# Optimization experiments

Hardware: AMD Instinct MI355X
Metric: run time of the kernel (lower is better)

## Reference

```python
import jax, jax.numpy as jnp
import numpy as np

TS = 0.1
ECNUM = 1024
CA1NUM = 1024
CA3NUM = 1024
CA3SIGMA = 5.0
TRACKLEN = 100
ACTNUM = 2
BS = 8192
CUELOC = int(0.1 * TRACKLEN)  # sensory cue injected at this step
NOISE_P = 0.04 * TS           # per-step EC3 spontaneous-spike probability


def _xavier_std(fan_in, fan_out):
    return float(np.sqrt(2.0 / (fan_in + fan_out)))


def setup_inputs() -> dict:
    key = jax.random.key(0)
    ks = jax.random.split(key, 6)
    cue = jax.random.normal(ks[0], (BS, ECNUM), jnp.float32)
    ec5_init = jax.random.uniform(ks[1], (BS, ECNUM), jnp.float32)
    wca3ca1 = jax.random.uniform(ks[2], (CA3NUM, CA1NUM), jnp.float32) * 0.01
    wec3ca1 = jax.random.normal(ks[3], (ECNUM, CA1NUM), jnp.float32) * _xavier_std(ECNUM, CA1NUM)
    wca1ec5 = jax.random.normal(ks[4], (CA1NUM, ECNUM), jnp.float32) * _xavier_std(CA1NUM, ECNUM)
    wca1act = jax.random.normal(ks[5], (CA1NUM, ACTNUM), jnp.float32) * _xavier_std(CA1NUM, ACTNUM)
    ca1bias = jnp.zeros((CA1NUM,), jnp.float32)
    ec5bias = jnp.zeros((ECNUM,), jnp.float32)
    actbias = jnp.zeros((ACTNUM,), jnp.float32)
    return {"cue": cue, "ec5_init": ec5_init, "wca3ca1": wca3ca1,
            "wec3ca1": wec3ca1, "wca1ec5": wca1ec5, "wca1act": wca1act,
            "ca1bias": ca1bias, "ec5bias": ec5bias, "actbias": actbias}


def _forward(cue, ec5_init, wca3ca1, wec3ca1, wca1ec5, wca1act, ca1bias, ec5bias, actbias):
    bs = cue.shape[0]
    dt = cue.dtype
    # CA3 place-cell tuning curves for all positions: (T, ca3num)
    ca3center = jnp.linspace(0.0, TRACKLEN, CA3NUM).astype(dt)
    xs = jnp.arange(TRACKLEN)
    ca3_all = jnp.exp(-((ca3center[None, :] - xs[:, None].astype(dt)) ** 2)
                      / (2.0 * CA3SIGMA ** 2))
    drive = ca3_all @ wca3ca1            # (T, ca1num), precomputed CA3->CA1 drive
    cue_mask = (xs == CUELOC).astype(dt)  # (T,)
    noise_key = jax.random.key(42)

    ec3_0 = jnp.zeros((bs, ECNUM), dt)
    ca1_0 = jnp.zeros((bs, CA1NUM), dt)

    def step(carry, inp):
        ec3, ec5, _ = carry
        d, m, t = inp
        ca1 = jax.nn.relu(d[None, :] * (1.0 + jax.nn.sigmoid(ec3 @ wec3ca1)) - ca1bias)
        ec5 = ec5 + (10.0 * TS) * (ca1 @ wca1ec5) + ec5bias
        ec5 = 0.5 + 0.5 * jax.nn.sigmoid(4.0 * (ec5 - 0.5))
        ec3 = ec5 * ec3 + m * cue
        k = jax.random.fold_in(noise_key, t)
        ec3 = ec3 + 0.2 * jax.random.bernoulli(k, NOISE_P, (bs, ECNUM)).astype(dt)
        return (ec3, ec5, ca1), None

    (ec3, ec5, ca1), _ = jax.lax.scan(step, (ec3_0, ec5_init, ca1_0),
                                      (drive, cue_mask, xs))
    return ca1 @ wca1act + actbias       # (bs, actnum)


def reference(cue, ec5_init, wca3ca1, wec3ca1, wca1ec5, wca1act, ca1bias, ec5bias, actbias):
    return _forward(cue, ec5_init, wca3ca1, wec3ca1, wca1ec5, wca1act,
                    ca1bias, ec5bias, actbias)
```

## Files before the change

### kernel.cpp

```cpp
#include <hip/hip_runtime.h>
#include <stdint.h>

#define BS 8192
#define NDIM 1024
#define T_STEPS 100
#define CUE_T 10
#define BK 64
#define NKT (NDIM / BK)

typedef __attribute__((ext_vector_type(8))) short bf16x8;
typedef __attribute__((ext_vector_type(16))) float f32x16;

__device__ inline uint16_t f32_to_bf16(float f) {
    uint32_t u = __float_as_uint(f);
    uint32_t r = u + 0x7fffu + ((u >> 16) & 1u);
    return (uint16_t)(r >> 16);
}
__device__ inline float bf16_to_f32(uint16_t h) {
    return __uint_as_float(((uint32_t)h) << 16);
}

__host__ __device__ inline uint32_t rotl32_(uint32_t x, uint32_t r) {
    return (x << r) | (x >> (32u - r));
}

__host__ __device__ inline void tf2x32(uint32_t k0, uint32_t k1,
                                       uint32_t x0, uint32_t x1,
                                       uint32_t &o0, uint32_t &o1) {
    uint32_t ks2 = k0 ^ k1 ^ 0x1BD11BDAu;
    x0 += k0; x1 += k1;
#define TF_R4(a,b,c,d) \
    x0 += x1; x1 = rotl32_(x1,(a)); x1 ^= x0; \
    x0 += x1; x1 = rotl32_(x1,(b)); x1 ^= x0; \
    x0 += x1; x1 = rotl32_(x1,(c)); x1 ^= x0; \
    x0 += x1; x1 = rotl32_(x1,(d)); x1 ^= x0;
    TF_R4(13,15,26,6)  x0 += k1;  x1 += ks2 + 1u;
    TF_R4(17,29,16,24) x0 += ks2; x1 += k0 + 2u;
    TF_R4(13,15,26,6)  x0 += k0;  x1 += k1 + 3u;
    TF_R4(17,29,16,24) x0 += k1;  x1 += ks2 + 4u;
    TF_R4(13,15,26,6)  x0 += ks2; x1 += k0 + 5u;
#undef TF_R4
    o0 = x0; o1 = x1;
}

__device__ inline float noise_add(uint32_t k0, uint32_t k1, uint32_t idx) {
    uint32_t o0, o1;
    tf2x32(k0, k1, 0u, idx, o0, o1);
    uint32_t bits = o0 ^ o1;
    float u = __uint_as_float((bits >> 9) | 0x3f800000u) - 1.0f;
    return (u < 0.004f) ? 0.2f : 0.0f;
}

__device__ inline float sigmoidf_(float x) {
    return 1.0f / (1.0f + expf(-x));
}

__device__ __forceinline__ void gload16(const uint16_t* g, uint16_t* l) {
    __builtin_amdgcn_global_load_lds(
        (const __attribute__((address_space(1))) void*)g,
        (__attribute__((address_space(3))) void*)l, 16, 0, 0);
}

__global__ void init_kernel(const float* __restrict__ ec5_init,
                            uint16_t* __restrict__ ec3bf,
                            uint16_t* __restrict__ ec5bf, int n) {
    int i = blockIdx.x * blockDim.x + threadIdx.x;
    if (i < n) { ec3bf[i] = 0; ec5bf[i] = f32_to_bf16(ec5_init[i]); }
}

__global__ __launch_bounds__(256) void drive_kernel(const float* __restrict__ W,
                                                    float* __restrict__ drive) {
    __shared__ float g[4][1024];
    const int t0 = blockIdx.x * 4;
    const int c = blockIdx.y * 256 + threadIdx.x;
    const float stepf = 100.0f / 1023.0f;
    for (int i = threadIdx.x; i < 4096; i += 256) {
        int tt = i >> 10, j = i & 1023;
        float d = stepf * (float)j - (float)(t0 + tt);
        g[tt][j] = expf(-(d * d) * 0.02f);
    }
    __syncthreads();
    float a0 = 0.f, a1 = 0.f, a2 = 0.f, a3 = 0.f;
    for (int j = 0; j < 1024; ++j) {
        float w = W[(size_t)j * NDIM + c];
        a0 = fmaf(g[0][j], w, a0);
        a1 = fmaf(g[1][j], w, a1);
        a2 = fmaf(g[2][j], w, a2);
        a3 = fmaf(g[3][j], w, a3);
    }
    drive[(size_t)(t0 + 0) * NDIM + c] = a0;
    drive[(size_t)(t0 + 1) * NDIM + c] = a1;
    drive[(size_t)(t0 + 2) * NDIM + c] = a2;
    drive[(size_t)(t0 + 3) * NDIM + c] = a3;
}

__global__ __launch_bounds__(256) void wtrans_kernel(const float* __restrict__ W,
                                                     uint16_t* __restrict__ Wt) {
    __shared__ float tile[32][33];
    int k0 = blockIdx.x * 32, n0 = blockIdx.y * 32;
    int tx = threadIdx.x & 31, ty = threadIdx.x >> 5;
    #pragma unroll
    for (int i = 0; i < 32; i += 8)
        tile[ty + i][tx] = W[(size_t)(k0 + ty + i) * NDIM + n0 + tx];
    __syncthreads();
    #pragma unroll
    for (int i = 0; i < 32; i += 8)
        Wt[(size_t)(n0 + ty + i) * NDIM + k0 + tx] = f32_to_bf16(tile[tx][ty + i]);
}

__device__ __forceinline__ void gemm_core(const uint16_t* __restrict__ A,
                                          const uint16_t* __restrict__ Bt,
                                          uint16_t* As, uint16_t* Bs,
                                          f32x16 acc[2][2]) {
    const int tid = threadIdx.x;
    const int wid = tid >> 6, lane = tid & 63;
    const int row0 = blockIdx.x * 128, col0 = blockIdx.y * 128;
    const int srow = lane >> 3;
    const int soff = ((lane & 7) ^ srow) * 8;
    const uint16_t* aS[4]; const uint16_t* bS[4];
    #pragma unroll
    for (int i = 0; i < 4; ++i) {
        int ch = wid * 4 + i;
        aS[i] = A  + (size_t)(row0 + ch * 8 + srow) * NDIM + soff;
        bS[i] = Bt + (size_t)(col0 + ch * 8 + srow) * NDIM + soff;
    }
    const int l31 = lane & 31, l5 = lane >> 5;
    const int wr = wid >> 1, wc = wid & 1;
    int aoff[2][4], boff[2][4];
    #pragma unroll
    for (int m = 0; m < 2; ++m)
        #pragma unroll
        for (int kk = 0; kk < 4; ++kk) {
            int ar = wr * 64 + m * 32 + l31;
            aoff[m][kk] = ar * BK + ((((kk << 1) | l5) ^ (ar & 7)) << 3);
            int br = wc * 64 + m * 32 + l31;
            boff[m][kk] = br * BK + ((((kk << 1) | l5) ^ (br & 7)) << 3);
        }

    #pragma unroll
    for (int i = 0; i < 4; ++i) {
        int ch = wid * 4 + i;
        gload16(aS[i], As + ch * 512);
        gload16(bS[i], Bs + ch * 512);
    }

    for (int kt = 0; kt < NKT; ++kt) {
        const int cur = kt & 1;
        if (kt + 1 < NKT) {
            const int nb = (cur ^ 1) * 8192;
            const int k0n = (kt + 1) * BK;
            #pragma unroll
            for (int i = 0; i < 4; ++i) {
                int ch = wid * 4 + i;
                gload16(aS[i] + k0n, As + nb + ch * 512);
                gload16(bS[i] + k0n, Bs + nb + ch * 512);
            }
            asm volatile("s_waitcnt vmcnt(8)" ::: "memory");
        } else {
            asm volatile("s_waitcnt vmcnt(0)" ::: "memory");
        }
        __builtin_amdgcn_s_barrier();
        __builtin_amdgcn_sched_barrier(0);
        const uint16_t* as = As + cur * 8192;
        const uint16_t* bs = Bs + cur * 8192;
        bf16x8 af[2][4], bfr[2][4];
        #pragma unroll
        for (int m = 0; m < 2; ++m)
            #pragma unroll
            for (int kk = 0; kk < 4; ++kk) {
                af[m][kk]  = *(const bf16x8*)&as[aoff[m][kk]];
                bfr[m][kk] = *(const bf16x8*)&bs[boff[m][kk]];
            }
        #pragma unroll
        for (int kk = 0; kk < 4; ++kk)
            #pragma unroll
            for (int m = 0; m < 2; ++m)
                #pragma unroll
                for (int n = 0; n < 2; ++n)
                    acc[m][n] = __builtin_amdgcn_mfma_f32_32x32x16_bf16(
                        af[m][kk], bfr[n][kk], acc[m][n], 0, 0, 0);
        __builtin_amdgcn_sched_barrier(0);
        __builtin_amdgcn_s_barrier();
    }
}

__device__ __forceinline__ void acc_to_lds(float* lacc, f32x16 acc[2][2]) {
    const int tid = threadIdx.x, wid = tid >> 6, lane = tid & 63;
    const int wr = wid >> 1, wc = wid & 1, l31 = lane & 31, l5 = lane >> 5;
    #pragma unroll
    for (int m = 0; m < 2; ++m)
        #pragma unroll
        for (int n = 0; n < 2; ++n) {
            int c = wc * 64 + n * 32 + l31;
            int chunk = c >> 2, cj = c & 3;
            #pragma unroll
            for (int e = 0; e < 16; ++e) {
                int r = wr * 64 + m * 32 + (e & 3) + ((e >> 2) << 3) + (l5 << 2);
                lacc[r * 128 + ((chunk ^ (r & 31)) << 2) + cj] = acc[m][n][e];
            }
        }
}

__device__ __forceinline__ void acc_read8(const float* lacc, int r, int a,
                                          float4 &v0, float4 &v1) {
    int rb = r & 31;
    v0 = *(const float4*)&lacc[r * 128 + ((((a << 1) | 0) ^ rb) << 2)];
    v1 = *(const float4*)&lacc[r * 128 + ((((a << 1) | 1) ^ rb) << 2)];
}

__global__ __launch_bounds__(256, 2) void gemm1_kernel(
    const uint16_t* __restrict__ ec3bf, const uint16_t* __restrict__ W1t,
    const float* __restrict__ drv, const float* __restrict__ bias,
    uint16_t* __restrict__ ca1bf, float* __restrict__ ca1f, int writef32)
{
    __shared__ __align__(16) uint16_t SM[2][16384];
    uint16_t* As = SM[0];
    uint16_t* Bs = SM[1];
    f32x16 acc[2][2];
    #pragma unroll
    for (int m = 0; m < 2; ++m)
        #pragma unroll
        for (int n = 0; n < 2; ++n)
            acc[m][n] = (f32x16)(0.0f);
    gemm_core(ec3bf, W1t, As, Bs, acc);

    float* lacc = (float*)SM;
    acc_to_lds(lacc, acc);
    __syncthreads();

    const int tid = threadIdx.x;
    const int row0 = blockIdx.x * 128, col0 = blockIdx.y * 128;
    const int a = tid & 15;
    #pragma unroll
    for (int i = 0; i < 8; ++i) {
        int r = (tid >> 4) + i * 16;
        float4 v0, v1;
        acc_read8(lacc, r, a, v0, v1);
        int gc = col0 + a * 8;
        float4 d0 = *(const float4*)&drv[gc];
        float4 d1 = *(const float4*)&drv[gc + 4];
        float4 b0 = *(const float4*)&bias[gc];
        float4 b1 = *(const float4*)&bias[gc + 4];
        size_t off = (size_t)(row0 + r) * NDIM + gc;
        float vout[8];
        #pragma unroll
        for (int j = 0; j < 8; ++j) {
            float accv = j < 4 ? v0[j] : v1[j - 4];
            float dv = j < 4 ? d0[j] : d1[j - 4];
            float bi = j < 4 ? b0[j] : b1[j - 4];
            float s = sigmoidf_(accv);
            float v = dv * (1.0f + s) - bi;
            vout[j] = v > 0.0f ? v : 0.0f;
        }
        bf16x8 pk;
        #pragma unroll
        for (int j = 0; j < 8; ++j) pk[j] = (short)f32_to_bf16(vout[j]);
        *(bf16x8*)&ca1bf[off] = pk;
        if (writef32) {
            float4 f0 = {vout[0], vout[1], vout[2], vout[3]};
            float4 f1 = {vout[4], vout[5], vout[6], vout[7]};
            *(float4*)&ca1f[off] = f0;
            *(float4*)&ca1f[off + 4] = f1;
        }
    }
}

__global__ __launch_bounds__(256, 2) void gemm2_kernel(
    const uint16_t* __restrict__ ca1bf, const uint16_t* __restrict__ W2t,
    const float* __restrict__ cue, const float* __restrict__ bias,
    uint16_t* __restrict__ ec3bf, uint16_t* __restrict__ ec5bf,
    uint32_t k0_, uint32_t k1_, int inject)
{
    __shared__ __align__(16) uint16_t SM[2][16384];
    uint16_t* As = SM[0];
    uint16_t* Bs = SM[1];
    f32x16 acc[2][2];
    #pragma unroll
    for (int m = 0; m < 2; ++m)
        #pragma unroll
        for (int n = 0; n < 2; ++n)
            acc[m][n] = (f32x16)(0.0f);
    gemm_core(ca1bf, W2t, As, Bs, acc);

    float* lacc = (float*)SM;
    acc_to_lds(lacc, acc);
    __syncthreads();

    const int tid = threadIdx.x;
    const int row0 = blockIdx.x * 128, col0 = blockIdx.y * 128;
    const int a = tid & 15;
    #pragma unroll
    for (int i = 0; i < 8; ++i) {
        int r = (tid >> 4) + i * 16;
        float4 v0, v1;
        acc_read8(lacc, r, a, v0, v1);
        int gc = col0 + a * 8;
        size_t off = (size_t)(row0 + r) * NDIM + gc;
        bf16x8 e3v = *(const bf16x8*)&ec3bf[off];
        bf16x8 e5v = *(const bf16x8*)&ec5bf[off];
        float4 b0 = *(const float4*)&bias[gc];
        float4 b1 = *(const float4*)&bias[gc + 4];
        float4 c0 = {0.f,0.f,0.f,0.f}, c1 = {0.f,0.f,0.f,0.f};
        if (inject) {
            c0 = *(const float4*)&cue[off];
            c1 = *(const float4*)&cue[off + 4];
        }
        bf16x8 p3, p5;
        #pragma unroll
        for (int j = 0; j < 8; ++j) {
            float accv = j < 4 ? v0[j] : v1[j - 4];
            float bi = j < 4 ? b0[j] : b1[j - 4];
            float e5 = bf16_to_f32((uint16_t)e5v[j]);
            float e3 = bf16_to_f32((uint16_t)e3v[j]);
            float u = e5 + accv + bi;
            float e5n = 0.5f + 0.5f * sigmoidf_(4.0f * (u - 0.5f));
            float e3n = e5n * e3;
            if (inject) e3n += (j < 4 ? c0[j] : c1[j - 4]);
            e3n += noise_add(k0_, k1_, (uint32_t)off + j);
            p5[j] = (short)f32_to_bf16(e5n);
            p3[j] = (short)f32_to_bf16(e3n);
        }
        *(bf16x8*)&ec5bf[off] = p5;
        *(bf16x8*)&ec3bf[off] = p3;
    }
}

__global__ __launch_bounds__(256) void final_kernel(
    const float* __restrict__ ca1,
    const float* __restrict__ wact,
    const float* __restrict__ actbias,
    float* __restrict__ out)
{
    int wave = threadIdx.x >> 6, lane = threadIdx.x & 63;
    int b = blockIdx.x * 4 + wave;
    double a0 = 0.0, a1 = 0.0;
    for (int c = lane; c < NDIM; c += 64) {
        double v = (double)ca1[(size_t)b * NDIM + c];
        a0 += v * (double)wact[c * 2 + 0];
        a1 += v * (double)wact[c * 2 + 1];
    }
    #pragma unroll
    for (int off = 32; off > 0; off >>= 1) {
        a0 += __shfl_down(a0, off);
        a1 += __shfl_down(a1, off);
    }
    if (lane == 0) {
        out[(size_t)b * 2 + 0] = (float)(a0 + (double)actbias[0]);
        out[(size_t)b * 2 + 1] = (float)(a1 + (double)actbias[1]);
    }
}

extern "C" void kernel_launch(void* const* d_in, const int* in_sizes, int n_in,
                              void* d_out, int out_size, void* d_ws, size_t ws_size,
                              hipStream_t stream) {
    const float* cue      = (const float*)d_in[0];
    const float* ec5_init = (const float*)d_in[1];
    const float* wca3ca1  = (const float*)d_in[2];
    const float* wec3ca1  = (const float*)d_in[3];
    const float* wca1ec5  = (const float*)d_in[4];
    const float* wca1act  = (const float*)d_in[5];
    const float* ca1bias  = (const float*)d_in[6];
    const float* ec5bias  = (const float*)d_in[7];
    const float* actbias  = (const float*)d_in[8];
    float* out = (float*)d_out;

    const size_t NE = (size_t)BS * NDIM;
    char* p = (char*)d_ws;
    float*    ca1f  = (float*)p;      p += NE * 4;
    uint16_t* ec3bf = (uint16_t*)p;   p += NE * 2;
    uint16_t* ec5bf = (uint16_t*)p;   p += NE * 2;
    uint16_t* ca1bf = (uint16_t*)p;   p += NE * 2;
    uint16_t* W1t   = (uint16_t*)p;   p += (size_t)NDIM * NDIM * 2;
    uint16_t* W2t   = (uint16_t*)p;   p += (size_t)NDIM * NDIM * 2;
    float*    drive = (float*)p;

    const int n = (int)NE;
    hipLaunchKernelGGL(init_kernel, dim3((n + 255) / 256), dim3(256), 0, stream,
                       ec5_init, ec3bf, ec5bf, n);
    hipLaunchKernelGGL(drive_kernel, dim3(25, 4), dim3(256), 0, stream,
                       wca3ca1, drive);
    hipLaunchKernelGGL(wtrans_kernel, dim3(32, 32), dim3(256), 0, stream, wec3ca1, W1t);
    hipLaunchKernelGGL(wtrans_kernel, dim3(32, 32), dim3(256), 0, stream, wca1ec5, W2t);

    dim3 blk(256);
    dim3 gg(BS / 128, NDIM / 128);
    for (int t = 0; t < T_STEPS; ++t) {
        hipLaunchKernelGGL(gemm1_kernel, gg, blk, 0, stream,
                           ec3bf, W1t, drive + (size_t)t * NDIM, ca1bias,
                           ca1bf, ca1f, (t == T_STEPS - 1) ? 1 : 0);
        if (t < T_STEPS - 1) {
            uint32_t k0, k1;
            tf2x32(0u, 42u, 0u, (uint32_t)t, k0, k1);
            hipLaunchKernelGGL(gemm2_kernel, gg, blk, 0, stream,
                               ca1bf, W2t, cue, ec5bias, ec3bf, ec5bf, k0, k1,
                               (t == CUE_T) ? 1 : 0);
        }
    }
    hipLaunchKernelGGL(final_kernel, dim3(BS / 4), blk, 0, stream,
                       ca1f, wca1act, actbias, out);
}
```

Before: 7.296 ms.

## Interleave Threefry noise generation with MFMA k-loop and prefetch ec state

The Threefry noise bits for gemm2's epilogue are now computed inside the GEMM k-loop, four elements per k-tile, and stored as a 64-bit mask. This lets the integer ALU work hide behind MFMA and load latency instead of running serially in the epilogue. The ec3/ec5 state loads are issued before the accumulator-to-LDS transfer so their latency overlaps. The fp32 ca1 copy is dropped and the final kernel reads the bf16 ca1 instead, which risks a small accuracy loss and adds register pressure from the mask and prefetched vectors.

```diff
diff --git a/kernel.cpp b/kernel.cpp
--- a/kernel.cpp
+++ b/kernel.cpp
@@ -43,14 +43,6 @@
     o0 = x0; o1 = x1;
 }
 
-__device__ inline float noise_add(uint32_t k0, uint32_t k1, uint32_t idx) {
-    uint32_t o0, o1;
-    tf2x32(k0, k1, 0u, idx, o0, o1);
-    uint32_t bits = o0 ^ o1;
-    float u = __uint_as_float((bits >> 9) | 0x3f800000u) - 1.0f;
-    return (u < 0.004f) ? 0.2f : 0.0f;
-}
-
 __device__ inline float sigmoidf_(float x) {
     return 1.0f / (1.0f + expf(-x));
 }
@@ -108,10 +100,13 @@
         Wt[(size_t)(n0 + ty + i) * NDIM + k0 + tx] = f32_to_bf16(tile[tx][ty + i]);
 }
 
-__device__ __forceinline__ void gemm_core(const uint16_t* __restrict__ A,
-                                          const uint16_t* __restrict__ Bt,
-                                          uint16_t* As, uint16_t* Bs,
-                                          f32x16 acc[2][2]) {
+template<bool NOISE>
+__device__ __forceinline__ void gemm_core_t(const uint16_t* __restrict__ A,
+                                            const uint16_t* __restrict__ Bt,
+                                            uint16_t* As, uint16_t* Bs,
+                                            f32x16 acc[2][2],
+                                            uint32_t k0_, uint32_t k1_,
+                                            uint32_t obase, uint64_t &mask) {
     const int tid = threadIdx.x;
     const int wid = tid >> 6, lane = tid & 63;
     const int row0 = blockIdx.x * 128, col0 = blockIdx.y * 128;
@@ -179,6 +174,18 @@
                 for (int n = 0; n < 2; ++n)
                     acc[m][n] = __builtin_amdgcn_mfma_f32_32x32x16_bf16(
                         af[m][kk], bfr[n][kk], acc[m][n], 0, 0, 0);
+        if (NOISE) {
+            #pragma unroll
+            for (int u = 0; u < 4; ++u) {
+                int e = (kt << 2) + u;
+                uint32_t off = obase + (uint32_t)((e >> 3) << 14) + (uint32_t)(e & 7);
+                uint32_t o0, o1;
+                tf2x32(k0_, k1_, 0u, off, o0, o1);
+                uint32_t bits = o0 ^ o1;
+                float uu = __uint_as_float((bits >> 9) | 0x3f800000u) - 1.0f;
+                mask |= (uint64_t)(uu < 0.004f ? 1u : 0u) << e;
+            }
+        }
         __builtin_amdgcn_sched_barrier(0);
         __builtin_amdgcn_s_barrier();
     }
@@ -211,7 +218,7 @@
 __global__ __launch_bounds__(256, 2) void gemm1_kernel(
     const uint16_t* __restrict__ ec3bf, const uint16_t* __restrict__ W1t,
     const float* __restrict__ drv, const float* __restrict__ bias,
-    uint16_t* __restrict__ ca1bf, float* __restrict__ ca1f, int writef32)
+    uint16_t* __restrict__ ca1bf)
 {
     __shared__ __align__(16) uint16_t SM[2][16384];
     uint16_t* As = SM[0];
@@ -222,7 +229,8 @@
         #pragma unroll
         for (int n = 0; n < 2; ++n)
             acc[m][n] = (f32x16)(0.0f);
-    gemm_core(ec3bf, W1t, As, Bs, acc);
+    uint64_t dummy = 0;
+    gemm_core_t<false>(ec3bf, W1t, As, Bs, acc, 0u, 0u, 0u, dummy);
 
     float* lacc = (float*)SM;
     acc_to_lds(lacc, acc);
@@ -242,7 +250,7 @@
         float4 b0 = *(const float4*)&bias[gc];
         float4 b1 = *(const float4*)&bias[gc + 4];
         size_t off = (size_t)(row0 + r) * NDIM + gc;
-        float vout[8];
+        bf16x8 pk;
         #pragma unroll
         for (int j = 0; j < 8; ++j) {
             float accv = j < 4 ? v0[j] : v1[j - 4];
@@ -250,18 +258,10 @@
             float bi = j < 4 ? b0[j] : b1[j - 4];
             float s = sigmoidf_(accv);
             float v = dv * (1.0f + s) - bi;
-            vout[j] = v > 0.0f ? v : 0.0f;
-        }
-        bf16x8 pk;
-        #pragma unroll
-        for (int j = 0; j < 8; ++j) pk[j] = (short)f32_to_bf16(vout[j]);
+            v = v > 0.0f ? v : 0.0f;
+            pk[j] = (short)f32_to_bf16(v);
+        }
         *(bf16x8*)&ca1bf[off] = pk;
-        if (writef32) {
-            float4 f0 = {vout[0], vout[1], vout[2], vout[3]};
-            float4 f1 = {vout[4], vout[5], vout[6], vout[7]};
-            *(float4*)&ca1f[off] = f0;
-            *(float4*)&ca1f[off + 4] = f1;
-        }
     }
 }
 
@@ -280,15 +280,27 @@
         #pragma unroll
         for (int n = 0; n < 2; ++n)
             acc[m][n] = (f32x16)(0.0f);
-    gemm_core(ca1bf, W2t, As, Bs, acc);
+
+    const int tid = threadIdx.x;
+    const int row0 = blockIdx.x * 128, col0 = blockIdx.y * 128;
+    const int a = tid & 15;
+    const uint32_t obase = (uint32_t)(row0 + (tid >> 4)) * NDIM
+                         + (uint32_t)(col0 + a * 8);
+    uint64_t mask = 0;
+    gemm_core_t<true>(ca1bf, W2t, As, Bs, acc, k0_, k1_, obase, mask);
+
+    bf16x8 e3v[8], e5v[8];
+    #pragma unroll
+    for (int i = 0; i < 8; ++i) {
+        size_t off = (size_t)(row0 + (tid >> 4) + i * 16) * NDIM + col0 + a * 8;
+        e3v[i] = *(const bf16x8*)&ec3bf[off];
+        e5v[i] = *(const bf16x8*)&ec5bf[off];
+    }
 
     float* lacc = (float*)SM;
     acc_to_lds(lacc, acc);
     __syncthreads();
 
-    const int tid = threadIdx.x;
-    const int row0 = blockIdx.x * 128, col0 = blockIdx.y * 128;
-    const int a = tid & 15;
     #pragma unroll
     for (int i = 0; i < 8; ++i) {
         int r = (tid >> 4) + i * 16;
@@ -296,8 +308,6 @@
         acc_read8(lacc, r, a, v0, v1);
         int gc = col0 + a * 8;
         size_t off = (size_t)(row0 + r) * NDIM + gc;
-        bf16x8 e3v = *(const bf16x8*)&ec3bf[off];
-        bf16x8 e5v = *(const bf16x8*)&ec5bf[off];
         float4 b0 = *(const float4*)&bias[gc];
         float4 b1 = *(const float4*)&bias[gc + 4];
         float4 c0 = {0.f,0.f,0.f,0.f}, c1 = {0.f,0.f,0.f,0.f};
@@ -310,13 +320,13 @@
         for (int j = 0; j < 8; ++j) {
             float accv = j < 4 ? v0[j] : v1[j - 4];
             float bi = j < 4 ? b0[j] : b1[j - 4];
-            float e5 = bf16_to_f32((uint16_t)e5v[j]);
-            float e3 = bf16_to_f32((uint16_t)e3v[j]);
+            float e5 = bf16_to_f32((uint16_t)e5v[i][j]);
+            float e3 = bf16_to_f32((uint16_t)e3v[i][j]);
             float u = e5 + accv + bi;
             float e5n = 0.5f + 0.5f * sigmoidf_(4.0f * (u - 0.5f));
             float e3n = e5n * e3;
             if (inject) e3n += (j < 4 ? c0[j] : c1[j - 4]);
-            e3n += noise_add(k0_, k1_, (uint32_t)off + j);
+            e3n += ((mask >> (i * 8 + j)) & 1ull) ? 0.2f : 0.0f;
             p5[j] = (short)f32_to_bf16(e5n);
             p3[j] = (short)f32_to_bf16(e3n);
         }
@@ -326,7 +336,7 @@
 }
 
 __global__ __launch_bounds__(256) void final_kernel(
-    const float* __restrict__ ca1,
+    const uint16_t* __restrict__ ca1bf,
     const float* __restrict__ wact,
     const float* __restrict__ actbias,
     float* __restrict__ out)
@@ -334,10 +344,16 @@
     int wave = threadIdx.x >> 6, lane = threadIdx.x & 63;
     int b = blockIdx.x * 4 + wave;
     double a0 = 0.0, a1 = 0.0;
-    for (int c = lane; c < NDIM; c += 64) {
-        double v = (double)ca1[(size_t)b * NDIM + c];
-        a0 += v * (double)wact[c * 2 + 0];
-        a1 += v * (double)wact[c * 2 + 1];
+    #pragma unroll
+    for (int ch = 0; ch < 2; ++ch) {
+        int c0 = ch * 512 + lane * 8;
+        bf16x8 v = *(const bf16x8*)&ca1bf[(size_t)b * NDIM + c0];
+        #pragma unroll
+        for (int k = 0; k < 8; ++k) {
+            double vf = (double)bf16_to_f32((uint16_t)v[k]);
+            a0 += vf * (double)wact[(c0 + k) * 2 + 0];
+            a1 += vf * (double)wact[(c0 + k) * 2 + 1];
+        }
     }
     #pragma unroll
     for (int off = 32; off > 0; off >>= 1) {
@@ -366,7 +382,6 @@
 
     const size_t NE = (size_t)BS * NDIM;
     char* p = (char*)d_ws;
-    float*    ca1f  = (float*)p;      p += NE * 4;
     uint16_t* ec3bf = (uint16_t*)p;   p += NE * 2;
     uint16_t* ec5bf = (uint16_t*)p;   p += NE * 2;
     uint16_t* ca1bf = (uint16_t*)p;   p += NE * 2;
@@ -386,8 +401,7 @@
     dim3 gg(BS / 128, NDIM / 128);
     for (int t = 0; t < T_STEPS; ++t) {
         hipLaunchKernelGGL(gemm1_kernel, gg, blk, 0, stream,
-                           ec3bf, W1t, drive + (size_t)t * NDIM, ca1bias,
-                           ca1bf, ca1f, (t == T_STEPS - 1) ? 1 : 0);
+                           ec3bf, W1t, drive + (size_t)t * NDIM, ca1bias, ca1bf);
         if (t < T_STEPS - 1) {
             uint32_t k0, k1;
             tf2x32(0u, 42u, 0u, (uint32_t)t, k0, k1);
@@ -397,5 +411,5 @@
         }
     }
     hipLaunchKernelGGL(final_kernel, dim3(BS / 4), blk, 0, stream,
-                       ca1f, wca1act, actbias, out);
-}
+                       ca1bf, wca1act, actbias, out);
+}
```

New measurement: 6.991 ms. 4.2% less time.
